# Performance work log

Hardware: AMD Instinct MI355X
Metric: run time of the kernel (lower is better)

## Reference

```python
import jax, jax.numpy as jnp
import numpy as np

B, C, H, W = 8, 256, 128, 128
EPS = 1e-12  # F.normalize eps


def setup_inputs() -> dict:
    key = jax.random.key(0)
    k0, k1, k2, k3 = jax.random.split(key, 4)
    x = jax.random.normal(k0, (B, C, H, W), jnp.float32)
    # qkv: Conv2d(C, 3C, 1, bias=False) -> weight [3C, C]
    w_qkv = jax.random.normal(k1, (3 * C, C), jnp.float32) * 0.02
    # qkv_dwconv: Conv2d(3C, 3C, 1, groups=3C) -> per-channel scale [3C]
    w_dw = jax.random.normal(k2, (3 * C,), jnp.float32) * 0.1 + 1.0
    # temperature: Parameter(ones(num_heads=1, 1, 1))
    temperature = jnp.ones((1, 1, 1), jnp.float32)
    # project_out: Conv2d(C, C, 1, bias=False) -> weight [C, C]
    w_proj = jax.random.normal(k3, (C, C), jnp.float32) * 0.02
    return {"x": x, "w_qkv": w_qkv, "w_dw": w_dw,
            "temperature": temperature, "w_proj": w_proj}


def reference(x, w_qkv, w_dw, temperature, w_proj):
    b, c, h, w = x.shape
    n = h * w
    # pointwise conv + depthwise 1x1 conv (= per-channel scale)
    qkv = jnp.einsum('bchw,oc->bohw', x, w_qkv) * w_dw[None, :, None, None]
    q, k, v = jnp.split(qkv, 3, axis=1)          # each [b, c, h, w]
    q = q.reshape(b, c, n)
    k = k.reshape(b, c, n)
    v = v.reshape(b, c, n)
    # L2-normalize along spatial dim (F.normalize: x / max(||x||, eps))
    q = q / jnp.maximum(jnp.linalg.norm(q, axis=-1, keepdims=True), EPS)
    k = k / jnp.maximum(jnp.linalg.norm(k, axis=-1, keepdims=True), EPS)
    # channel-wise cosine attention: [b, c, c]
    attn = jnp.einsum('bcn,bdn->bcd', q, k) * temperature[0]
    attn = jax.nn.softmax(attn, axis=-1)
    out = jnp.einsum('bcd,bdn->bcn', attn, v).reshape(b, c, h, w)
    out = jnp.einsum('bchw,oc->bohw', out, w_proj)
    return out
```

## Files before the change

kernel.cpp:

```cpp
#include <hip/hip_runtime.h>
#include <hip/hip_bf16.h>
#include <stdint.h>

#define NB 8
#define NC 256
#define NN 16384
#define KS 32

typedef short bf16x8 __attribute__((ext_vector_type(8)));
typedef float f32x4  __attribute__((ext_vector_type(4)));
typedef uint32_t u32;

__device__ __forceinline__ unsigned short f2bf(float f) {
  union { float f; unsigned u; } c; c.f = f;
  return (unsigned short)((c.u + 0x7FFFu + ((c.u >> 16) & 1u)) >> 16);
}
__device__ __forceinline__ float bf2f(unsigned short h) {
  union { unsigned u; float f; } c; c.u = ((unsigned)h) << 16;
  return c.f;
}
__device__ __forceinline__ u32 pk2(float a, float b) {
  union { __hip_bfloat162 h; u32 u; } c;
  c.h = __float22bfloat162_rn(make_float2(a, b));
  return c.u;
}

__device__ __forceinline__ void gload16(const void* g, void* l) {
  __builtin_amdgcn_global_load_lds(
      (const __attribute__((address_space(1))) u32*)g,
      (__attribute__((address_space(3))) u32*)l, 16, 0, 0);
}

__device__ __forceinline__ void stage_tile(const char* src, int ld_bytes,
                                           char* lds, int w, int l) {
#pragma unroll
  for (int i = 0; i < 4; ++i) {
    int s = (w * 4 + i) * 64 + l;
    int row = s >> 3;
    int srcslot = (l & 7) ^ (row & 7);
    gload16(src + (size_t)row * ld_bytes + srcslot * 16,
            lds + (w * 4 + i) * 1024);
  }
}

__global__ __launch_bounds__(1024) void k_gramT(
    const float* __restrict__ x, unsigned short* __restrict__ gpart,
    char* __restrict__ xt,
    const float* __restrict__ wqkv, const float* __restrict__ wdw,
    float* __restrict__ Wcat, float* __restrict__ WkT,
    float* __restrict__ Wv2) {
  __shared__ __align__(16) unsigned short tile[256 * 72];
  const int bid = blockIdx.x;
  const int tid = threadIdx.x;

  if (bid >= KS * NB) {
    const int r = (bid - KS * NB) * 4 + (tid >> 8);
    const int t = tid & 255;
    Wcat[r * 256 + t] = wqkv[r * 256 + t] * wdw[r];
    float kv = wqkv[(256 + r) * 256 + t] * wdw[256 + r];
    Wcat[65536 + r * 256 + t] = kv;
    WkT[t * 256 + r] = kv;
    Wv2[r * 256 + t] = wqkv[(512 + r) * 256 + t] * wdw[512 + r];
    return;
  }

  const int ks = bid & (KS - 1), b = bid >> 5;
  const int w = tid >> 6, l = tid & 63;
  const int wm = w >> 2, wn = w & 3;
  const int cg = tid >> 4, ng = tid & 15;
  const int c0 = cg * 4, n0 = ng * 4;
  f32x4 acc[4][4];
#pragma unroll
  for (int m = 0; m < 4; ++m)
#pragma unroll
    for (int n = 0; n < 4; ++n) acc[m][n] = (f32x4){0.f, 0.f, 0.f, 0.f};
  const float* x0 = x + (size_t)b * NC * NN + (size_t)ks * 512;

  float4 f[4];
  u32 hw[4][2];

#define LOADS(kt)                                                           \
  {                                                                         \
    _Pragma("unroll") for (int j = 0; j < 4; ++j)                           \
        f[j] = *(const float4*)&x0[(size_t)(c0 + j) * NN + (kt) * 64 + n0]; \
  }
#define CVT()                                                               \
  {                                                                         \
    _Pragma("unroll") for (int j = 0; j < 4; ++j) {                         \
      hw[j][0] = pk2(f[j].x, f[j].y);                                       \
      hw[j][1] = pk2(f[j].z, f[j].w);                                       \
    }                                                                       \
  }
#define DSW()                                                               \
  {                                                                         \
    _Pragma("unroll") for (int j = 0; j < 4; ++j)                           \
        *(uint2*)&tile[(c0 + j) * 72 + n0] = make_uint2(hw[j][0], hw[j][1]);\
  }

  LOADS(0); CVT(); DSW();
  __syncthreads();

  for (int kt = 0; kt < 8; ++kt) {
    if (kt < 7) LOADS(kt + 1);
#pragma unroll
    for (int ks2 = 0; ks2 < 2; ++ks2) {
      const int ko = ks2 * 32 + (l >> 4) * 8;
      bf16x8 av[4], bv[4];
#pragma unroll
      for (int m = 0; m < 4; ++m) {
        int row = wm * 64 + m * 16 + (l & 15);
        av[m] = *(const bf16x8*)&tile[row * 72 + ko];
      }
#pragma unroll
      for (int n = 0; n < 4; ++n) {
        int row = wn * 64 + n * 16 + (l & 15);
        bv[n] = *(const bf16x8*)&tile[row * 72 + ko];
      }
#pragma unroll
      for (int m = 0; m < 4; ++m)
#pragma unroll
        for (int n = 0; n < 4; ++n)
          acc[m][n] = __builtin_amdgcn_mfma_f32_16x16x32_bf16(
              av[m], bv[n], acc[m][n], 0, 0, 0);
    }
    {
      const int gn = ks * 512 + kt * 64 + n0;
#pragma unroll
      for (int k = 0; k < 4; ++k) {
        u32 e0 = (k < 2) ? (hw[0][0] >> (16 * k)) : (hw[0][1] >> (16 * (k - 2)));
        u32 e1 = (k < 2) ? (hw[1][0] >> (16 * k)) : (hw[1][1] >> (16 * (k - 2)));
        u32 e2 = (k < 2) ? (hw[2][0] >> (16 * k)) : (hw[2][1] >> (16 * (k - 2)));
        u32 e3 = (k < 2) ? (hw[3][0] >> (16 * k)) : (hw[3][1] >> (16 * (k - 2)));
        uint2 ov = make_uint2((e0 & 0xffff) | (e1 << 16),
                              (e2 & 0xffff) | (e3 << 16));
        *(uint2*)(xt + (((size_t)b * NN + gn + k) * 256 + c0) * 2) = ov;
      }
    }
    __syncthreads();
    if (kt < 7) {
      CVT();
      DSW();
      __syncthreads();
    }
  }
#undef LOADS
#undef CVT
#undef DSW
  unsigned short* gp = gpart + ((size_t)(ks * NB + b)) * 65536;
#pragma unroll
  for (int m = 0; m < 4; ++m)
#pragma unroll
    for (int n = 0; n < 4; ++n)
#pragma unroll
      for (int r = 0; r < 4; ++r) {
        int c = wm * 64 + m * 16 + ((l >> 4) << 2) + r;
        int d = wn * 64 + n * 16 + (l & 15);
        gp[(size_t)c * 256 + d] = f2bf(acc[m][n][r]);
      }
}

__global__ __launch_bounds__(256) void k_reduceG(
    const unsigned short* __restrict__ gpart, float* __restrict__ G) {
  const int t = threadIdx.x;
  const int c = blockIdx.x * 2 + (t >> 7), b = blockIdx.y;
  const int d0 = (t & 127) * 2;
  float s0 = 0.f, s1 = 0.f;
#pragma unroll 8
  for (int ks = 0; ks < KS; ++ks) {
    u32 v = *(const u32*)(gpart + (((size_t)ks * NB + b) * 256 + c) * 256 + d0);
    s0 += bf2f((unsigned short)(v & 0xffff));
    s1 += bf2f((unsigned short)(v >> 16));
  }
  *(float2*)(G + ((size_t)b * 256 + c) * 256 + d0) = make_float2(s0, s1);
}

__global__ __launch_bounds__(256) void k_sgT(const float* __restrict__ Wcat,
                                             const float* __restrict__ G,
                                             float* __restrict__ T12,
                                             float* __restrict__ nqk) {
  const int t = threadIdx.x;
  const int r0 = blockIdx.x * 8, b = blockIdx.y;
  const float* Gb = G + (size_t)b * 65536 + t;
  float acc[8] = {0, 0, 0, 0, 0, 0, 0, 0};
#pragma unroll 4
  for (int k = 0; k < 256; ++k) {
    float bv = Gb[(size_t)k * 256];
#pragma unroll
    for (int o = 0; o < 8; ++o) acc[o] += Wcat[(r0 + o) * 256 + k] * bv;
  }
#pragma unroll
  for (int o = 0; o < 8; ++o)
    T12[(size_t)b * 131072 + (size_t)(r0 + o) * 256 + t] = acc[o];
  __shared__ float red[8][4];
  const int w = t >> 6, l = t & 63;
#pragma unroll
  for (int o = 0; o < 8; ++o) {
    float s = acc[o] * Wcat[(r0 + o) * 256 + t];
#pragma unroll
    for (int off = 32; off; off >>= 1) s += __shfl_xor(s, off);
    if (l == 0) red[o][w] = s;
  }
  __syncthreads();
  if (t < 8)
    nqk[b * 512 + r0 + t] = red[t][0] + red[t][1] + red[t][2] + red[t][3];
}

__global__ __launch_bounds__(256) void k_ssoft(const float* __restrict__ T12,
                                               const float* __restrict__ WkT,
                                               const float* __restrict__ nqk,
                                               const float* __restrict__ temp,
                                               float* __restrict__ attn) {
  const int t = threadIdx.x;
  const int c0 = blockIdx.x * 8, b = blockIdx.y;
  const float* Ab = T12 + (size_t)b * 131072 + (size_t)c0 * 256;
  const float* Bb = WkT + t;
  float acc[8] = {0, 0, 0, 0, 0, 0, 0, 0};
#pragma unroll 4
  for (int k = 0; k < 256; ++k) {
    float bv = Bb[(size_t)k * 256];
#pragma unroll
    for (int o = 0; o < 8; ++o) acc[o] += Ab[o * 256 + k] * bv;
  }
  const float rk = 1.0f / fmaxf(sqrtf(fmaxf(nqk[b * 512 + 256 + t], 0.f)), 1e-12f);
  const float tau = temp[0];
#pragma unroll
  for (int o = 0; o < 8; ++o) {
    float rq = 1.0f / fmaxf(sqrtf(fmaxf(nqk[b * 512 + c0 + o], 0.f)), 1e-12f);
    acc[o] = acc[o] * rq * rk * tau;
  }
  __shared__ float redm[8][4];
  __shared__ float reds[8][4];
  const int w = t >> 6, l = t & 63;
#pragma unroll
  for (int o = 0; o < 8; ++o) {
    float m = acc[o];
#pragma unroll
    for (int off = 32; off; off >>= 1) m = fmaxf(m, __shfl_xor(m, off));
    if (l == 0) redm[o][w] = m;
  }
  __syncthreads();
  float e[8];
#pragma unroll
  for (int o = 0; o < 8; ++o) {
    float m = fmaxf(fmaxf(redm[o][0], redm[o][1]), fmaxf(redm[o][2], redm[o][3]));
    e[o] = __expf(acc[o] - m);
    float s = e[o];
#pragma unroll
    for (int off = 32; off; off >>= 1) s += __shfl_xor(s, off);
    if (l == 0) reds[o][w] = s;
  }
  __syncthreads();
#pragma unroll
  for (int o = 0; o < 8; ++o) {
    float tot = reds[o][0] + reds[o][1] + reds[o][2] + reds[o][3];
    attn[(size_t)b * 65536 + (size_t)(c0 + o) * 256 + t] = e[o] / tot;
  }
}

__global__ __launch_bounds__(256) void k_sg2x(const float* __restrict__ wp,
                                              const float* __restrict__ attn,
                                              const float* __restrict__ wv2,
                                              char* __restrict__ Fb) {
  __shared__ float P[8 * 256];
  const int t = threadIdx.x;
  const int o0 = blockIdx.x * 8, b = blockIdx.y;
  const float* Ab = wp + (size_t)o0 * 256;
  const float* Bb = attn + (size_t)b * 65536 + t;
  float acc[8] = {0, 0, 0, 0, 0, 0, 0, 0};
#pragma unroll 4
  for (int k = 0; k < 256; ++k) {
    float bv = Bb[(size_t)k * 256];
#pragma unroll
    for (int o = 0; o < 8; ++o) acc[o] += Ab[o * 256 + k] * bv;
  }
#pragma unroll
  for (int o = 0; o < 8; ++o) P[o * 256 + t] = acc[o];
  __syncthreads();
  float a2[8] = {0, 0, 0, 0, 0, 0, 0, 0};
  const float* Bv = wv2 + t;
#pragma unroll 4
  for (int k = 0; k < 256; ++k) {
    float bv = Bv[(size_t)k * 256];
#pragma unroll
    for (int o = 0; o < 8; ++o) a2[o] += P[o * 256 + k] * bv;
  }
  unsigned short* Cp = (unsigned short*)Fb + (size_t)b * 65536;
#pragma unroll
  for (int o = 0; o < 8; ++o) Cp[(size_t)(o0 + o) * 256 + t] = f2bf(a2[o]);
}

__global__ __launch_bounds__(256) void k_final(const char* __restrict__ xt,
                                               const char* __restrict__ fb,
                                               float* __restrict__ out) {
  __shared__ char smem[65536];
  const int tid = threadIdx.x;
  const int nt = blockIdx.x, ot = blockIdx.y, b = blockIdx.z;
  const int w = tid >> 6, l = tid & 63;
  const int wm = w >> 1, wn = w & 1;
  f32x4 acc[4][4];
#pragma unroll
  for (int m = 0; m < 4; ++m)
#pragma unroll
    for (int nq = 0; nq < 4; ++nq) acc[m][nq] = (f32x4){0.f, 0.f, 0.f, 0.f};
  const char* Ap = xt + ((size_t)b * NN + (size_t)nt * 128) * 512;
  const char* Bp = fb + ((size_t)(b * 256 + ot * 128)) * 512;

  stage_tile(Ap, 512, smem, w, l);
  stage_tile(Bp, 512, smem + 16384, w, l);
  __syncthreads();
  for (int kt = 0; kt < 4; ++kt) {
    if (kt < 3) {
      char* nb = smem + ((kt + 1) & 1) * 32768;
      stage_tile(Ap + (kt + 1) * 128, 512, nb, w, l);
      stage_tile(Bp + (kt + 1) * 128, 512, nb + 16384, w, l);
    }
    const char* As = smem + (kt & 1) * 32768;
    const char* Bs = As + 16384;
#pragma unroll
    for (int ks = 0; ks < 2; ++ks) {
      bf16x8 av[4], bv[4];
      const int kb = ks * 64 + ((l >> 4) << 4);
#pragma unroll
      for (int m = 0; m < 4; ++m) {
        int row = wm * 64 + m * 16 + (l & 15);
        av[m] = *(const bf16x8*)(As + row * 128 + (kb ^ ((row & 7) << 4)));
      }
#pragma unroll
      for (int nq = 0; nq < 4; ++nq) {
        int row = wn * 64 + nq * 16 + (l & 15);
        bv[nq] = *(const bf16x8*)(Bs + row * 128 + (kb ^ ((row & 7) << 4)));
      }
#pragma unroll
      for (int m = 0; m < 4; ++m)
#pragma unroll
        for (int nq = 0; nq < 4; ++nq)
          acc[m][nq] = __builtin_amdgcn_mfma_f32_16x16x32_bf16(
              av[m], bv[nq], acc[m][nq], 0, 0, 0);
    }
    __syncthreads();
  }
#pragma unroll
  for (int m = 0; m < 4; ++m)
#pragma unroll
    for (int nq = 0; nq < 4; ++nq)
#pragma unroll
      for (int r = 0; r < 4; ++r) {
        int i = wm * 64 + m * 16 + ((l >> 4) << 2) + r;
        int j = wn * 64 + nq * 16 + (l & 15);
        *(float*)(smem + j * 512 + ((i * 4) ^ ((j & 7) << 4))) = acc[m][nq][r];
      }
  __syncthreads();
  const int j = tid >> 1, h = tid & 1;
  float* dst = out + ((size_t)(b * 256 + ot * 128 + j)) * NN + nt * 128;
#pragma unroll
  for (int cc = 0; cc < 16; ++cc) {
    int ch = h * 16 + cc;
    *(uint4*)(dst + ch * 4) =
        *(const uint4*)(smem + j * 512 + ((ch * 16) ^ ((j & 7) << 4)));
  }
}

extern "C" void kernel_launch(void* const* d_in, const int* in_sizes, int n_in,
                              void* d_out, int out_size, void* d_ws, size_t ws_size,
                              hipStream_t stream) {
  const float* x     = (const float*)d_in[0];
  const float* wqkv  = (const float*)d_in[1];
  const float* wdwf  = (const float*)d_in[2];
  const float* temp  = (const float*)d_in[3];
  const float* wproj = (const float*)d_in[4];
  float* out = (float*)d_out;
  char* ws = (char*)d_ws;

  char*  xt    = ws;
  unsigned short* gpart = (unsigned short*)(ws + 67108864);
  float* G     = (float*)(ws + 100663296);
  float* T12   = (float*)(ws + 102760448);
  float* attn  = (float*)(ws + 106954752);
  char*  Fb    = ws + 109051904;
  float* Wcat  = (float*)(ws + 110100480);
  float* WkT   = (float*)(ws + 110624768);
  float* Wv2   = (float*)(ws + 110886912);
  float* nqk   = (float*)(ws + 111149056);

  k_gramT<<<dim3(KS * NB + 64), dim3(1024), 0, stream>>>(
      x, gpart, xt, wqkv, wdwf, Wcat, WkT, Wv2);
  k_reduceG<<<dim3(128, NB), dim3(256), 0, stream>>>(gpart, G);
  k_sgT<<<dim3(64, NB), dim3(256), 0, stream>>>(Wcat, G, T12, nqk);
  k_ssoft<<<dim3(32, NB), dim3(256), 0, stream>>>(T12, WkT, nqk, temp, attn);
  k_sg2x<<<dim3(32, NB), dim3(256), 0, stream>>>(wproj, attn, Wv2, Fb);
  k_final<<<dim3(128, 2, NB), dim3(256), 0, stream>>>(xt, Fb, out);
}
```

Measured before the change: 232.4 us.

## Double Gram split-K blocks and simplify k_final staging and epilogue

```diff
diff --git a/kernel.cpp b/kernel.cpp
--- a/kernel.cpp
+++ b/kernel.cpp
@@ -5,7 +5,7 @@
 #define NB 8
 #define NC 256
 #define NN 16384
-#define KS 32
+#define KS 64
 
 typedef short bf16x8 __attribute__((ext_vector_type(8)));
 typedef float f32x4  __attribute__((ext_vector_type(4)));
@@ -64,7 +64,7 @@
     return;
   }
 
-  const int ks = bid & (KS - 1), b = bid >> 5;
+  const int ks = bid & (KS - 1), b = bid >> 6;
   const int w = tid >> 6, l = tid & 63;
   const int wm = w >> 2, wn = w & 3;
   const int cg = tid >> 4, ng = tid & 15;
@@ -74,7 +74,7 @@
   for (int m = 0; m < 4; ++m)
 #pragma unroll
     for (int n = 0; n < 4; ++n) acc[m][n] = (f32x4){0.f, 0.f, 0.f, 0.f};
-  const float* x0 = x + (size_t)b * NC * NN + (size_t)ks * 512;
+  const float* x0 = x + (size_t)b * NC * NN + (size_t)ks * 256;
 
   float4 f[4];
   u32 hw[4][2];
@@ -100,8 +100,8 @@
   LOADS(0); CVT(); DSW();
   __syncthreads();
 
-  for (int kt = 0; kt < 8; ++kt) {
-    if (kt < 7) LOADS(kt + 1);
+  for (int kt = 0; kt < 4; ++kt) {
+    if (kt < 3) LOADS(kt + 1);
 #pragma unroll
     for (int ks2 = 0; ks2 < 2; ++ks2) {
       const int ko = ks2 * 32 + (l >> 4) * 8;
@@ -124,7 +124,7 @@
               av[m], bv[n], acc[m][n], 0, 0, 0);
     }
     {
-      const int gn = ks * 512 + kt * 64 + n0;
+      const int gn = ks * 256 + kt * 64 + n0;
 #pragma unroll
       for (int k = 0; k < 4; ++k) {
         u32 e0 = (k < 2) ? (hw[0][0] >> (16 * k)) : (hw[0][1] >> (16 * (k - 2)));
@@ -137,7 +137,7 @@
       }
     }
     __syncthreads();
-    if (kt < 7) {
+    if (kt < 3) {
       CVT();
       DSW();
       __syncthreads();
@@ -292,7 +292,7 @@
 __global__ __launch_bounds__(256) void k_final(const char* __restrict__ xt,
                                                const char* __restrict__ fb,
                                                float* __restrict__ out) {
-  __shared__ char smem[65536];
+  __shared__ char smem[32768];
   const int tid = threadIdx.x;
   const int nt = blockIdx.x, ot = blockIdx.y, b = blockIdx.z;
   const int w = tid >> 6, l = tid & 63;
@@ -305,17 +305,10 @@
   const char* Ap = xt + ((size_t)b * NN + (size_t)nt * 128) * 512;
   const char* Bp = fb + ((size_t)(b * 256 + ot * 128)) * 512;
 
-  stage_tile(Ap, 512, smem, w, l);
-  stage_tile(Bp, 512, smem + 16384, w, l);
-  __syncthreads();
   for (int kt = 0; kt < 4; ++kt) {
-    if (kt < 3) {
-      char* nb = smem + ((kt + 1) & 1) * 32768;
-      stage_tile(Ap + (kt + 1) * 128, 512, nb, w, l);
-      stage_tile(Bp + (kt + 1) * 128, 512, nb + 16384, w, l);
-    }
-    const char* As = smem + (kt & 1) * 32768;
-    const char* Bs = As + 16384;
+    stage_tile(Ap + kt * 128, 512, smem, w, l);
+    stage_tile(Bp + kt * 128, 512, smem + 16384, w, l);
+    __syncthreads();
 #pragma unroll
     for (int ks = 0; ks < 2; ++ks) {
       bf16x8 av[4], bv[4];
@@ -323,12 +316,13 @@
 #pragma unroll
       for (int m = 0; m < 4; ++m) {
         int row = wm * 64 + m * 16 + (l & 15);
-        av[m] = *(const bf16x8*)(As + row * 128 + (kb ^ ((row & 7) << 4)));
+        av[m] = *(const bf16x8*)(smem + row * 128 + (kb ^ ((row & 7) << 4)));
       }
 #pragma unroll
       for (int nq = 0; nq < 4; ++nq) {
         int row = wn * 64 + nq * 16 + (l & 15);
-        bv[nq] = *(const bf16x8*)(Bs + row * 128 + (kb ^ ((row & 7) << 4)));
+        bv[nq] = *(const bf16x8*)(smem + 16384 + row * 128 +
+                                  (kb ^ ((row & 7) << 4)));
       }
 #pragma unroll
       for (int m = 0; m < 4; ++m)
@@ -342,22 +336,11 @@
 #pragma unroll
   for (int m = 0; m < 4; ++m)
 #pragma unroll
-    for (int nq = 0; nq < 4; ++nq)
-#pragma unroll
-      for (int r = 0; r < 4; ++r) {
-        int i = wm * 64 + m * 16 + ((l >> 4) << 2) + r;
-        int j = wn * 64 + nq * 16 + (l & 15);
-        *(float*)(smem + j * 512 + ((i * 4) ^ ((j & 7) << 4))) = acc[m][nq][r];
-      }
-  __syncthreads();
-  const int j = tid >> 1, h = tid & 1;
-  float* dst = out + ((size_t)(b * 256 + ot * 128 + j)) * NN + nt * 128;
-#pragma unroll
-  for (int cc = 0; cc < 16; ++cc) {
-    int ch = h * 16 + cc;
-    *(uint4*)(dst + ch * 4) =
-        *(const uint4*)(smem + j * 512 + ((ch * 16) ^ ((j & 7) << 4)));
-  }
+    for (int nq = 0; nq < 4; ++nq) {
+      int o = ot * 128 + wn * 64 + nq * 16 + (l & 15);
+      int n = nt * 128 + wm * 64 + m * 16 + ((l >> 4) << 2);
+      *(f32x4*)(out + ((size_t)(b * 256 + o)) * NN + n) = acc[m][nq];
+    }
 }
 
 extern "C" void kernel_launch(void* const* d_in, const int* in_sizes, int n_in,
@@ -373,14 +356,14 @@
 
   char*  xt    = ws;
   unsigned short* gpart = (unsigned short*)(ws + 67108864);
-  float* G     = (float*)(ws + 100663296);
-  float* T12   = (float*)(ws + 102760448);
-  float* attn  = (float*)(ws + 106954752);
-  char*  Fb    = ws + 109051904;
-  float* Wcat  = (float*)(ws + 110100480);
-  float* WkT   = (float*)(ws + 110624768);
-  float* Wv2   = (float*)(ws + 110886912);
-  float* nqk   = (float*)(ws + 111149056);
+  float* G     = (float*)(ws + 134217728);
+  float* T12   = (float*)(ws + 136314880);
+  float* attn  = (float*)(ws + 140509184);
+  char*  Fb    = ws + 142606336;
+  float* Wcat  = (float*)(ws + 143654912);
+  float* WkT   = (float*)(ws + 144179200);
+  float* Wv2   = (float*)(ws + 144441344);
+  float* nqk   = (float*)(ws + 144703488);
 
   k_gramT<<<dim3(KS * NB + 64), dim3(1024), 0, stream>>>(
       x, gpart, xt, wqkv, wdwf, Wcat, WkT, Wv2);
```

Result: no change. 233.6 us (+0.5%).
